# Performance work log

Hardware: AMD Instinct MI355X
Metric: run time of the kernel (lower is better)

## Reference

```python
import jax, jax.numpy as jnp
import numpy as np

N, F, P, E, HID = 50000, 4, 12, 1_600_000, 64  # nodes, input feats, periods (FH), edges, hidden


def setup_inputs() -> dict:
    key = jax.random.key(0)
    ks = jax.random.split(key, 16)

    def nrm(k, shp, scale=0.1):
        return jax.random.normal(k, shp, jnp.float32) * scale

    inp = {
        "x": jax.random.normal(ks[0], (N, F, P), jnp.float32),
        "edge_index": jax.random.randint(ks[1], (2, E), 0, N),
        "edge_weights": jax.random.uniform(ks[2], (E,), jnp.float32),
        "att": nrm(ks[3], (P,), 1.0),
    }
    i = 4
    for g in ("z", "r", "h"):  # TGCN gate params: GCNConv weight/bias + Linear(2*hid, hid)
        inp[f"Wg_{g}"] = nrm(ks[i], (F, HID))
        inp[f"bg_{g}"] = jnp.zeros((HID,), jnp.float32)
        inp[f"Wl_{g}"] = nrm(jax.random.fold_in(ks[i], 1), (2 * HID, HID))
        inp[f"bl_{g}"] = jnp.zeros((HID,), jnp.float32)
        i += 1
    for j in range(1, 5):
        inp[f"W{j}"] = nrm(ks[i], (HID, HID))
        inp[f"b{j}"] = jnp.zeros((HID,), jnp.float32)
        i += 1
    inp["Wo"] = nrm(ks[i], (HID, P * F))
    inp["bo"] = jnp.zeros((P * F,), jnp.float32)
    return inp


def _gcn_norm(edge_index, ew):
    # GCNConv default: add self loops (weight 1), symmetric D^-1/2 (A+I) D^-1/2 normalization
    src, dst = edge_index[0], edge_index[1]
    loop = jnp.arange(N)
    src_f = jnp.concatenate([src, loop])
    dst_f = jnp.concatenate([dst, loop])
    ew_f = jnp.concatenate([ew, jnp.ones((N,), ew.dtype)])
    deg = jax.ops.segment_sum(ew_f, dst_f, num_segments=N)
    dinv = jnp.where(deg > 0, jax.lax.rsqrt(deg), 0.0)
    norm = dinv[src_f] * ew_f * dinv[dst_f]
    return src_f, dst_f, norm


def _gcn(x, W, b, src, dst, norm):
    xw = x @ W                               # [N, HID] transform before propagate
    msg = xw[src] * norm[:, None]            # gather + scale, [E+N, HID]
    return jax.ops.segment_sum(msg, dst, num_segments=N) + b


def reference(x, edge_index, edge_weights, att,
              Wg_z, bg_z, Wl_z, bl_z,
              Wg_r, bg_r, Wl_r, bl_r,
              Wg_h, bg_h, Wl_h, bl_h,
              W1, b1, W2, b2, W3, b3, W4, b4, Wo, bo):
    src, dst, norm = _gcn_norm(edge_index, edge_weights)

    def tgcn_cell(xt):
        # A3TGCN passes H=None every period -> H starts at zeros each period
        Hz = jnp.zeros((xt.shape[0], HID), xt.dtype)
        z = jax.nn.sigmoid(jnp.concatenate([_gcn(xt, Wg_z, bg_z, src, dst, norm), Hz], -1) @ Wl_z + bl_z)
        r = jax.nn.sigmoid(jnp.concatenate([_gcn(xt, Wg_r, bg_r, src, dst, norm), Hz], -1) @ Wl_r + bl_r)
        htil = jnp.tanh(jnp.concatenate([_gcn(xt, Wg_h, bg_h, src, dst, norm), Hz * r], -1) @ Wl_h + bl_h)
        return z * Hz + (1.0 - z) * htil

    probs = jax.nn.softmax(att)
    h = jnp.zeros((N, HID), x.dtype)
    for p in range(P):  # small fixed period loop keeps peak memory at one period's messages
        h = h + probs[p] * tgcn_cell(x[:, :, p])

    h = jax.nn.relu(h)
    h = h @ W1 + b1
    h = h @ W2 + b2
    h = h @ W3 + b3
    h = h @ W4 + b4
    h = h @ Wo + bo                          # [N, FH*F]
    return h.reshape(-1, F, P)
```

## Files before the change

### kernel.cpp

```cpp
#include <hip/hip_runtime.h>
#include <hip/hip_fp16.h>

#define FP 48
#define HID 64
#define NP 12
#define PL 65
#define NBLK 256
#define CAPB 9216

__device__ __forceinline__ void mm_stage(const float* __restrict__ Alds,
                                         const float* __restrict__ Wg,
                                         float* __restrict__ Clds, int t)
{
    const int rg = (t >> 4) * 4, cg = (t & 15) * 4;
    float acc[4][4] = {};
    for (int k = 0; k < 64; ++k) {
        float a0 = Alds[(rg + 0) * PL + k];
        float a1 = Alds[(rg + 1) * PL + k];
        float a2 = Alds[(rg + 2) * PL + k];
        float a3 = Alds[(rg + 3) * PL + k];
        const float4 bv = *reinterpret_cast<const float4*>(Wg + k * 64 + cg);
        acc[0][0] += a0 * bv.x; acc[0][1] += a0 * bv.y; acc[0][2] += a0 * bv.z; acc[0][3] += a0 * bv.w;
        acc[1][0] += a1 * bv.x; acc[1][1] += a1 * bv.y; acc[1][2] += a1 * bv.z; acc[1][3] += a1 * bv.w;
        acc[2][0] += a2 * bv.x; acc[2][1] += a2 * bv.y; acc[2][2] += a2 * bv.z; acc[2][3] += a2 * bv.w;
        acc[3][0] += a3 * bv.x; acc[3][1] += a3 * bv.y; acc[3][2] += a3 * bv.z; acc[3][3] += a3 * bv.w;
    }
    for (int i = 0; i < 4; ++i)
        for (int j = 0; j < 4; ++j)
            Clds[(rg + i) * PL + cg + j] = acc[i][j];
}

__device__ __forceinline__ void bias_stage(const float* __restrict__ bin,
                                           const float* __restrict__ Wg,
                                           const float* __restrict__ badd,
                                           float* __restrict__ bout, int t)
{
    if (t < 64) {
        float s = badd[t];
        for (int k = 0; k < 64; ++k) s += bin[k] * Wg[k * 64 + t];
        bout[t] = s;
    }
}

__device__ void do_prep(
    const float* __restrict__ att,
    const float* __restrict__ Wg_z, const float* __restrict__ bg_z,
    const float* __restrict__ Wl_z, const float* __restrict__ bl_z,
    const float* __restrict__ Wg_h, const float* __restrict__ bg_h,
    const float* __restrict__ Wl_h, const float* __restrict__ bl_h,
    const float* __restrict__ W1, const float* __restrict__ b1,
    const float* __restrict__ W2, const float* __restrict__ b2,
    const float* __restrict__ W3, const float* __restrict__ b3,
    const float* __restrict__ W4, const float* __restrict__ b4,
    const float* __restrict__ Wo, const float* __restrict__ bo,
    float* __restrict__ probs, float* __restrict__ Mz, float* __restrict__ cz,
    float* __restrict__ Mh, float* __restrict__ ch,
    float* __restrict__ Wc, float* __restrict__ bc, int t)
{
    __shared__ float A[64 * PL];
    __shared__ float B[64 * PL];
    __shared__ float bias[64];
    __shared__ float bias2[64];

    if (t == 0) {
        float m = att[0];
        for (int p = 1; p < NP; ++p) m = fmaxf(m, att[p]);
        float e[NP]; float s = 0.f;
        for (int p = 0; p < NP; ++p) { e[p] = __expf(att[p] - m); s += e[p]; }
        float inv = 1.f / s;
        for (int p = 0; p < NP; ++p) probs[p] = e[p] * inv;
    }

    {
        int f = t >> 6, j = t & 63;
        float az = 0.f, ah = 0.f;
        for (int k = 0; k < HID; ++k) {
            az += Wg_z[f * HID + k] * Wl_z[k * HID + j];
            ah += Wg_h[f * HID + k] * Wl_h[k * HID + j];
        }
        Mz[t] = az; Mh[t] = ah;
    }
    if (t < HID) {
        float az = bl_z[t], ah = bl_h[t];
        for (int k = 0; k < HID; ++k) {
            az += bg_z[k] * Wl_z[k * HID + t];
            ah += bg_h[k] * Wl_h[k * HID + t];
        }
        cz[t] = az; ch[t] = ah;
    }

    for (int idx = t; idx < 4096; idx += 256) {
        int i = idx >> 6, j = idx & 63;
        A[i * PL + j] = W1[idx];
    }
    if (t < 64) bias[t] = b1[t];
    __syncthreads();

    mm_stage(A, W2, B, t);
    bias_stage(bias, W2, b2, bias2, t);
    __syncthreads();
    mm_stage(B, W3, A, t);
    bias_stage(bias2, W3, b3, bias, t);
    __syncthreads();
    mm_stage(A, W4, B, t);
    bias_stage(bias, W4, b4, bias2, t);
    __syncthreads();

    const int rg = (t >> 4) * 4, cg = (t & 15) * 4;
    if (cg < FP) {
        float acc[4][4] = {};
        for (int k = 0; k < 64; ++k) {
            float a0 = B[(rg + 0) * PL + k];
            float a1 = B[(rg + 1) * PL + k];
            float a2 = B[(rg + 2) * PL + k];
            float a3 = B[(rg + 3) * PL + k];
            const float4 bv = *reinterpret_cast<const float4*>(Wo + k * FP + cg);
            acc[0][0] += a0 * bv.x; acc[0][1] += a0 * bv.y; acc[0][2] += a0 * bv.z; acc[0][3] += a0 * bv.w;
            acc[1][0] += a1 * bv.x; acc[1][1] += a1 * bv.y; acc[1][2] += a1 * bv.z; acc[1][3] += a1 * bv.w;
            acc[2][0] += a2 * bv.x; acc[2][1] += a2 * bv.y; acc[2][2] += a2 * bv.z; acc[2][3] += a2 * bv.w;
            acc[3][0] += a3 * bv.x; acc[3][1] += a3 * bv.y; acc[3][2] += a3 * bv.z; acc[3][3] += a3 * bv.w;
        }
        for (int i = 0; i < 4; ++i)
            for (int j = 0; j < 4; ++j)
                Wc[(rg + i) * FP + cg + j] = acc[i][j];
    }
    if (t < FP) {
        float s = bo[t];
        for (int k = 0; k < 64; ++k) s += bias2[k] * Wo[k * FP + t];
        bc[t] = s;
    }
}

__global__ __launch_bounds__(256) void build_kernel(
    const int* __restrict__ src, const int* __restrict__ dst,
    const float* __restrict__ ew,
    unsigned* __restrict__ cursor, int2* __restrict__ binned,
    int E, int CE, int NBUK,
    const float* __restrict__ att,
    const float* __restrict__ Wg_z, const float* __restrict__ bg_z,
    const float* __restrict__ Wl_z, const float* __restrict__ bl_z,
    const float* __restrict__ Wg_h, const float* __restrict__ bg_h,
    const float* __restrict__ Wl_h, const float* __restrict__ bl_h,
    const float* __restrict__ W1, const float* __restrict__ b1,
    const float* __restrict__ W2, const float* __restrict__ b2,
    const float* __restrict__ W3, const float* __restrict__ b3,
    const float* __restrict__ W4, const float* __restrict__ b4,
    const float* __restrict__ Wo, const float* __restrict__ bo,
    float* __restrict__ probs, float* __restrict__ Mz, float* __restrict__ cz,
    float* __restrict__ Mh, float* __restrict__ ch,
    float* __restrict__ Wc, float* __restrict__ bc)
{
    const int t = threadIdx.x;
    if (blockIdx.x == NBLK) {
        do_prep(att, Wg_z, bg_z, Wl_z, bl_z, Wg_h, bg_h, Wl_h, bl_h,
                W1, b1, W2, b2, W3, b3, W4, b4, Wo, bo,
                probs, Mz, cz, Mh, ch, Wc, bc, t);
        return;
    }
    __shared__ int cnt[256];
    __shared__ int off[256];
    for (int i = t; i < NBUK; i += 256) cnt[i] = 0;
    __syncthreads();
    const int base = blockIdx.x * CE;
    const int endb = min(base + CE, E);
    for (int e = base + t; e < endb; e += 256)
        atomicAdd(&cnt[((unsigned)dst[e]) >> 8], 1);
    __syncthreads();
    for (int i = t; i < NBUK; i += 256)
        off[i] = (int)atomicAdd(&cursor[i], (unsigned)cnt[i]);
    __syncthreads();
    for (int e = base + t; e < endb; e += 256) {
        const int d = dst[e];
        const int b = ((unsigned)d) >> 8;
        const int r = atomicAdd(&off[b], 1);
        if (r < CAPB)
            binned[(size_t)b * CAPB + r] =
                make_int2(((d & 255) << 16) | src[e], __float_as_int(ew[e]));
    }
}

__global__ __launch_bounds__(256) void csr_convert_kernel(
    const int2* __restrict__ binned, const unsigned* __restrict__ cursor,
    unsigned* __restrict__ csr, int2* __restrict__ nodeinfo,
    const float* __restrict__ x,
    unsigned short* __restrict__ xs, int N, int NBUK)
{
    const int t = threadIdx.x;
    const int b = blockIdx.x;
    const int node0 = b << 8;
    const int nend = min(256, N - node0);
    const int ebeg = b * CAPB;
    const int ecnt = min((int)cursor[b], CAPB);
    const int eend = ebeg + ecnt;

    __shared__ int   cnt[256];
    __shared__ float fsum[256];
    __shared__ int   pfx[256];
    __shared__ float sdi[256];

    cnt[t] = 0; fsum[t] = 0.f;
    __syncthreads();

    for (int e = ebeg + t; e < eend; e += 256) {
        const int2 v = binned[e];
        const int dl = (v.x >> 16) & 255;
        atomicAdd(&cnt[dl], 1);
        atomicAdd(&fsum[dl], __int_as_float(v.y));
    }
    __syncthreads();

    const int myc = cnt[t];
    pfx[t] = myc;
    __syncthreads();
    for (int off = 1; off < 256; off <<= 1) {
        int tmp = (t >= off) ? pfx[t - off] : 0;
        __syncthreads();
        pfx[t] += tmp;
        __syncthreads();
    }
    const int excl = pfx[t] - myc;

    const float di = rsqrtf(1.f + fsum[t]);
    sdi[t] = di;
    if (t < nend)
        nodeinfo[node0 + t] = make_int2((myc << 22) | (ebeg + excl), __float_as_int(di));

    cnt[t] = ebeg + excl;
    __syncthreads();

    for (int e = ebeg + t; e < eend; e += 256) {
        const int2 v = binned[e];
        const int dl = (v.x >> 16) & 255;
        const int pos = atomicAdd(&cnt[dl], 1);
        const float w = __int_as_float(v.y);
        const unsigned hb = (unsigned)__half_as_ushort(__float2half_rn(w));
        csr[pos] = (unsigned)(v.x & 0xffff) | (hb << 16);
    }

    const int gtot = nend * 6;
    for (int g = t; g < gtot; g += 256) {
        const int nl = g / 6;
        const int q = g - nl * 6;
        const float dsc = sdi[nl];
        const float* xr = x + (size_t)(node0 + nl) * FP + q * 8;
        const float4 v0 = *reinterpret_cast<const float4*>(xr);
        const float4 v1 = *reinterpret_cast<const float4*>(xr + 4);
        unsigned p0 = (unsigned)__half_as_ushort(__float2half_rn(dsc * v0.x)) |
                      ((unsigned)__half_as_ushort(__float2half_rn(dsc * v0.y)) << 16);
        unsigned p1 = (unsigned)__half_as_ushort(__float2half_rn(dsc * v0.z)) |
                      ((unsigned)__half_as_ushort(__float2half_rn(dsc * v0.w)) << 16);
        unsigned p2 = (unsigned)__half_as_ushort(__float2half_rn(dsc * v1.x)) |
                      ((unsigned)__half_as_ushort(__float2half_rn(dsc * v1.y)) << 16);
        unsigned p3 = (unsigned)__half_as_ushort(__float2half_rn(dsc * v1.z)) |
                      ((unsigned)__half_as_ushort(__float2half_rn(dsc * v1.w)) << 16);
        *reinterpret_cast<int4*>(xs + (size_t)(node0 + nl) * FP + q * 8) =
            make_int4((int)p0, (int)p1, (int)p2, (int)p3);
    }
}

__global__ __launch_bounds__(256) void gather_node_kernel(
    const unsigned short* __restrict__ xs, const float* __restrict__ x,
    const int2* __restrict__ nodeinfo,
    const unsigned* __restrict__ csr,
    const float* __restrict__ probs,
    const float* __restrict__ Mz, const float* __restrict__ cz,
    const float* __restrict__ Mh, const float* __restrict__ ch,
    const float* __restrict__ Wc, const float* __restrict__ bc,
    float* __restrict__ out, int N)
{
    __shared__ __align__(16) float sWc[HID * FP];
    __shared__ __align__(16) float sprobs[16];
    __shared__ __align__(16) float yacc[4][384];
    __shared__ __align__(16) float yld[4][FP];
    __shared__ __align__(16) float hld[4][HID];
    for (int i = threadIdx.x; i < HID * FP; i += 256) sWc[i] = Wc[i];
    if (threadIdx.x < NP) sprobs[threadIdx.x] = probs[threadIdx.x];
    __syncthreads();

    const int lane = threadIdx.x & 63;
    const int wib  = threadIdx.x >> 6;
    const int n    = blockIdx.x * 4 + wib;
    if (n >= N) return;

    const int slot = lane >> 3;
    const int q    = lane & 7;
    const bool act = (q < 6);
    const int qc   = act ? q : 5;
    const char* xsb = (const char*)xs;

    const int2 ni = nodeinfo[n];
    const int beg = ni.x & 0x3FFFFF;
    const int end = beg + ((unsigned)ni.x >> 22);
    const float di = __int_as_float(ni.y);

    float a0 = 0.f, a1 = 0.f, a2 = 0.f, a3 = 0.f;
    float a4 = 0.f, a5 = 0.f, a6 = 0.f, a7 = 0.f;
    #pragma unroll 2
    for (int e = beg + slot; e < end; e += 8) {
        const unsigned ev = csr[e];
        const float w = __half2float(__ushort_as_half((unsigned short)(ev >> 16)));
        const unsigned soff = (ev & 0xffffu) * 96u;
        const int4 xv = *reinterpret_cast<const int4*>(xsb + soff + (qc << 4));
        const float2 f0 = __half22float2(*reinterpret_cast<const __half2*>(&xv.x));
        const float2 f1 = __half22float2(*reinterpret_cast<const __half2*>(&xv.y));
        const float2 f2 = __half22float2(*reinterpret_cast<const __half2*>(&xv.z));
        const float2 f3 = __half22float2(*reinterpret_cast<const __half2*>(&xv.w));
        a0 = fmaf(w, f0.x, a0); a1 = fmaf(w, f0.y, a1);
        a2 = fmaf(w, f1.x, a2); a3 = fmaf(w, f1.y, a3);
        a4 = fmaf(w, f2.x, a4); a5 = fmaf(w, f2.y, a5);
        a6 = fmaf(w, f3.x, a6); a7 = fmaf(w, f3.y, a7);
    }

    if (act) {
        float* dst0 = &yacc[wib][slot * 48 + q * 8];
        *reinterpret_cast<float4*>(dst0)     = make_float4(a0, a1, a2, a3);
        *reinterpret_cast<float4*>(dst0 + 4) = make_float4(a4, a5, a6, a7);
    }

    if (lane < FP) {
        const float* yf = yacc[wib];
        float s = 0.f;
        #pragma unroll
        for (int sl = 0; sl < 8; ++sl) s += yf[sl * 48 + lane];
        float xself = x[(size_t)n * FP + lane];
        float yv = di * s + di * di * xself;
        int f = lane / 12;
        int p = lane - f * 12;
        yld[wib][p * 4 + f] = yv;
    }

    const float mz0 = Mz[lane], mz1 = Mz[64 + lane], mz2 = Mz[128 + lane], mz3 = Mz[192 + lane];
    const float mh0 = Mh[lane], mh1 = Mh[64 + lane], mh2 = Mh[128 + lane], mh3 = Mh[192 + lane];
    const float czv = cz[lane], chv = ch[lane];
    const int   c   = (lane < FP) ? lane : 0;
    const float bcv = bc[c];

    const float* yw = yld[wib];
    float hacc = 0.f;
    #pragma unroll
    for (int p = 0; p < NP; ++p) {
        const float4 v = *reinterpret_cast<const float4*>(yw + p * 4);
        float az = czv + v.x * mz0 + v.y * mz1 + v.z * mz2 + v.w * mz3;
        float ah = chv + v.x * mh0 + v.y * mh1 + v.z * mh2 + v.w * mh3;
        float g  = __builtin_amdgcn_rcpf(1.f + __expf(az));
        float ahc = fminf(fmaxf(ah, -15.f), 15.f);
        float eh = __expf(2.f * ahc);
        float th = 1.f - 2.f * __builtin_amdgcn_rcpf(eh + 1.f);
        hacc += sprobs[p] * g * th;
    }
    hacc = fmaxf(hacc, 0.f);

    hld[wib][lane] = hacc;
    const float* hw = hld[wib];
    float o = bcv;
    #pragma unroll
    for (int i4 = 0; i4 < 16; ++i4) {
        const float4 h4 = *reinterpret_cast<const float4*>(hw + i4 * 4);
        o += h4.x * sWc[(i4 * 4 + 0) * FP + c];
        o += h4.y * sWc[(i4 * 4 + 1) * FP + c];
        o += h4.z * sWc[(i4 * 4 + 2) * FP + c];
        o += h4.w * sWc[(i4 * 4 + 3) * FP + c];
    }
    if (lane < FP) out[(size_t)n * FP + lane] = o;
}

extern "C" void kernel_launch(void* const* d_in, const int* in_sizes, int n_in,
                              void* d_out, int out_size, void* d_ws, size_t ws_size,
                              hipStream_t stream)
{
    const int N = in_sizes[0] / FP;
    const int E = in_sizes[1] / 2;
    const int NBUK = (N + 255) >> 8;
    const int CE = (E + NBLK - 1) / NBLK;

    const float* x    = (const float*)d_in[0];
    const int*   ei   = (const int*)d_in[1];
    const float* ew   = (const float*)d_in[2];
    const float* att  = (const float*)d_in[3];
    const float* Wg_z = (const float*)d_in[4];
    const float* bg_z = (const float*)d_in[5];
    const float* Wl_z = (const float*)d_in[6];
    const float* bl_z = (const float*)d_in[7];
    const float* Wg_h = (const float*)d_in[12];
    const float* bg_h = (const float*)d_in[13];
    const float* Wl_h = (const float*)d_in[14];
    const float* bl_h = (const float*)d_in[15];
    const float* W1 = (const float*)d_in[16]; const float* b1 = (const float*)d_in[17];
    const float* W2 = (const float*)d_in[18]; const float* b2 = (const float*)d_in[19];
    const float* W3 = (const float*)d_in[20]; const float* b3 = (const float*)d_in[21];
    const float* W4 = (const float*)d_in[22]; const float* b4 = (const float*)d_in[23];
    const float* Wo = (const float*)d_in[24]; const float* bo = (const float*)d_in[25];

    const int* srcp = ei;
    const int* dstp = ei + E;

    int2* binned       = (int2*)d_ws;
    unsigned* csr      = (unsigned*)(binned + (size_t)NBUK * CAPB);
    unsigned short* xs = (unsigned short*)(csr + (size_t)NBUK * CAPB);
    unsigned* cursor   = (unsigned*)(xs + (size_t)N * FP);
    int2* nodeinfo     = (int2*)(cursor + 256);
    float* probs       = (float*)(nodeinfo + N);
    float* Mz          = probs + 16;
    float* cz          = Mz + 256;
    float* Mh          = cz + 64;
    float* ch          = Mh + 256;
    float* Wc          = ch + 64;
    float* bc          = Wc + HID * FP;

    hipMemsetAsync(cursor, 0, (size_t)NBUK * sizeof(unsigned), stream);

    build_kernel<<<NBLK + 1, 256, 0, stream>>>(
        srcp, dstp, ew, cursor, binned, E, CE, NBUK,
        att, Wg_z, bg_z, Wl_z, bl_z, Wg_h, bg_h, Wl_h, bl_h,
        W1, b1, W2, b2, W3, b3, W4, b4, Wo, bo,
        probs, Mz, cz, Mh, ch, Wc, bc);

    csr_convert_kernel<<<NBUK, 256, 0, stream>>>(binned, cursor, csr, nodeinfo,
                                                 x, xs, N, NBUK);

    gather_node_kernel<<<(N + 3) / 4, 256, 0, stream>>>(xs, x, nodeinfo, csr,
                                                        probs, Mz, cz, Mh, ch, Wc, bc,
                                                        (float*)d_out, N);
}
```

Measured before the change: 252.2 us.

## Widen edge binning and CSR convert grids, use fma_mix in gather loop

The edge-binning kernel now runs over 1024 blocks instead of 256, and skips cursor atomics for empty buckets. The CSR-convert kernel runs 1024 threads per block, with the per-node scan limited to the first 256 threads. The gather loop replaces separate half-to-float conversions with inline v_fma_mix_f32 instructions that multiply packed fp16 features by the fp16 edge weight directly. These changes aim to raise parallelism in the preprocessing stages, since CSR convert has only about 196 blocks, and to cut ALU work per edge. In exchange there are more global cursor atomics and inline assembly that depends on the target ISA.

```diff
diff --git a/kernel.cpp b/kernel.cpp
--- a/kernel.cpp
+++ b/kernel.cpp
@@ -5,7 +5,7 @@
 #define HID 64
 #define NP 12
 #define PL 65
-#define NBLK 256
+#define NBB 1024
 #define CAPB 9216
 
 __device__ __forceinline__ void mm_stage(const float* __restrict__ Alds,
@@ -151,7 +151,7 @@
     float* __restrict__ Wc, float* __restrict__ bc)
 {
     const int t = threadIdx.x;
-    if (blockIdx.x == NBLK) {
+    if (blockIdx.x == NBB) {
         do_prep(att, Wg_z, bg_z, Wl_z, bl_z, Wg_h, bg_h, Wl_h, bl_h,
                 W1, b1, W2, b2, W3, b3, W4, b4, Wo, bo,
                 probs, Mz, cz, Mh, ch, Wc, bc, t);
@@ -159,15 +159,17 @@
     }
     __shared__ int cnt[256];
     __shared__ int off[256];
-    for (int i = t; i < NBUK; i += 256) cnt[i] = 0;
-    __syncthreads();
     const int base = blockIdx.x * CE;
     const int endb = min(base + CE, E);
+    cnt[t] = 0;
+    __syncthreads();
     for (int e = base + t; e < endb; e += 256)
         atomicAdd(&cnt[((unsigned)dst[e]) >> 8], 1);
     __syncthreads();
-    for (int i = t; i < NBUK; i += 256)
-        off[i] = (int)atomicAdd(&cursor[i], (unsigned)cnt[i]);
+    if (t < NBUK) {
+        const int c = cnt[t];
+        off[t] = c ? (int)atomicAdd(&cursor[t], (unsigned)c) : 0;
+    }
     __syncthreads();
     for (int e = base + t; e < endb; e += 256) {
         const int d = dst[e];
@@ -179,7 +181,7 @@
     }
 }
 
-__global__ __launch_bounds__(256) void csr_convert_kernel(
+__global__ __launch_bounds__(1024) void csr_convert_kernel(
     const int2* __restrict__ binned, const unsigned* __restrict__ cursor,
     unsigned* __restrict__ csr, int2* __restrict__ nodeinfo,
     const float* __restrict__ x,
@@ -198,10 +200,10 @@
     __shared__ int   pfx[256];
     __shared__ float sdi[256];
 
-    cnt[t] = 0; fsum[t] = 0.f;
-    __syncthreads();
-
-    for (int e = ebeg + t; e < eend; e += 256) {
+    if (t < 256) { cnt[t] = 0; fsum[t] = 0.f; }
+    __syncthreads();
+
+    for (int e = ebeg + t; e < eend; e += 1024) {
         const int2 v = binned[e];
         const int dl = (v.x >> 16) & 255;
         atomicAdd(&cnt[dl], 1);
@@ -209,26 +211,27 @@
     }
     __syncthreads();
 
-    const int myc = cnt[t];
-    pfx[t] = myc;
+    const int myc = (t < 256) ? cnt[t] : 0;
+    if (t < 256) pfx[t] = myc;
     __syncthreads();
     for (int off = 1; off < 256; off <<= 1) {
-        int tmp = (t >= off) ? pfx[t - off] : 0;
+        int tmp = (t >= off && t < 256) ? pfx[t - off] : 0;
         __syncthreads();
-        pfx[t] += tmp;
+        if (t < 256) pfx[t] += tmp;
         __syncthreads();
     }
-    const int excl = pfx[t] - myc;
-
-    const float di = rsqrtf(1.f + fsum[t]);
-    sdi[t] = di;
-    if (t < nend)
-        nodeinfo[node0 + t] = make_int2((myc << 22) | (ebeg + excl), __float_as_int(di));
-
-    cnt[t] = ebeg + excl;
-    __syncthreads();
-
-    for (int e = ebeg + t; e < eend; e += 256) {
+
+    if (t < 256) {
+        const int excl = pfx[t] - myc;
+        const float di = rsqrtf(1.f + fsum[t]);
+        sdi[t] = di;
+        if (t < nend)
+            nodeinfo[node0 + t] = make_int2((myc << 22) | (ebeg + excl), __float_as_int(di));
+        cnt[t] = ebeg + excl;
+    }
+    __syncthreads();
+
+    for (int e = ebeg + t; e < eend; e += 1024) {
         const int2 v = binned[e];
         const int dl = (v.x >> 16) & 255;
         const int pos = atomicAdd(&cnt[dl], 1);
@@ -238,7 +241,7 @@
     }
 
     const int gtot = nend * 6;
-    for (int g = t; g < gtot; g += 256) {
+    for (int g = t; g < gtot; g += 1024) {
         const int nl = g / 6;
         const int q = g - nl * 6;
         const float dsc = sdi[nl];
@@ -258,6 +261,13 @@
     }
 }
 
+#define FMAMIX_LO(acc, xpk, evw) \
+    asm("v_fma_mix_f32 %0, %1, %2, %0 op_sel:[0,1,0] op_sel_hi:[1,1,0]" \
+        : "+v"(acc) : "v"(xpk), "v"(evw))
+#define FMAMIX_HI(acc, xpk, evw) \
+    asm("v_fma_mix_f32 %0, %1, %2, %0 op_sel:[1,1,0] op_sel_hi:[1,1,0]" \
+        : "+v"(acc) : "v"(xpk), "v"(evw))
+
 __global__ __launch_bounds__(256) void gather_node_kernel(
     const unsigned short* __restrict__ xs, const float* __restrict__ x,
     const int2* __restrict__ nodeinfo,
@@ -290,7 +300,7 @@
 
     const int2 ni = nodeinfo[n];
     const int beg = ni.x & 0x3FFFFF;
-    const int end = beg + ((unsigned)ni.x >> 22);
+    const int end = beg + (int)((unsigned)ni.x >> 22);
     const float di = __int_as_float(ni.y);
 
     float a0 = 0.f, a1 = 0.f, a2 = 0.f, a3 = 0.f;
@@ -298,17 +308,12 @@
     #pragma unroll 2
     for (int e = beg + slot; e < end; e += 8) {
         const unsigned ev = csr[e];
-        const float w = __half2float(__ushort_as_half((unsigned short)(ev >> 16)));
         const unsigned soff = (ev & 0xffffu) * 96u;
         const int4 xv = *reinterpret_cast<const int4*>(xsb + soff + (qc << 4));
-        const float2 f0 = __half22float2(*reinterpret_cast<const __half2*>(&xv.x));
-        const float2 f1 = __half22float2(*reinterpret_cast<const __half2*>(&xv.y));
-        const float2 f2 = __half22float2(*reinterpret_cast<const __half2*>(&xv.z));
-        const float2 f3 = __half22float2(*reinterpret_cast<const __half2*>(&xv.w));
-        a0 = fmaf(w, f0.x, a0); a1 = fmaf(w, f0.y, a1);
-        a2 = fmaf(w, f1.x, a2); a3 = fmaf(w, f1.y, a3);
-        a4 = fmaf(w, f2.x, a4); a5 = fmaf(w, f2.y, a5);
-        a6 = fmaf(w, f3.x, a6); a7 = fmaf(w, f3.y, a7);
+        FMAMIX_LO(a0, xv.x, ev); FMAMIX_HI(a1, xv.x, ev);
+        FMAMIX_LO(a2, xv.y, ev); FMAMIX_HI(a3, xv.y, ev);
+        FMAMIX_LO(a4, xv.z, ev); FMAMIX_HI(a5, xv.z, ev);
+        FMAMIX_LO(a6, xv.w, ev); FMAMIX_HI(a7, xv.w, ev);
     }
 
     if (act) {
@@ -371,7 +376,7 @@
     const int N = in_sizes[0] / FP;
     const int E = in_sizes[1] / 2;
     const int NBUK = (N + 255) >> 8;
-    const int CE = (E + NBLK - 1) / NBLK;
+    const int CE = (E + NBB - 1) / NBB;
 
     const float* x    = (const float*)d_in[0];
     const int*   ei   = (const int*)d_in[1];
@@ -409,14 +414,14 @@
 
     hipMemsetAsync(cursor, 0, (size_t)NBUK * sizeof(unsigned), stream);
 
-    build_kernel<<<NBLK + 1, 256, 0, stream>>>(
+    build_kernel<<<NBB + 1, 256, 0, stream>>>(
         srcp, dstp, ew, cursor, binned, E, CE, NBUK,
         att, Wg_z, bg_z, Wl_z, bl_z, Wg_h, bg_h, Wl_h, bl_h,
         W1, b1, W2, b2, W3, b3, W4, b4, Wo, bo,
         probs, Mz, cz, Mh, ch, Wc, bc);
 
-    csr_convert_kernel<<<NBUK, 256, 0, stream>>>(binned, cursor, csr, nodeinfo,
-                                                 x, xs, N, NBUK);
+    csr_convert_kernel<<<NBUK, 1024, 0, stream>>>(binned, cursor, csr, nodeinfo,
+                                                  x, xs, N, NBUK);
 
     gather_node_kernel<<<(N + 3) / 4, 256, 0, stream>>>(xs, x, nodeinfo, csr,
                                                         probs, Mz, cz, Mh, ch, Wc, bc,
```

Result: slower. 273.8 us (+8.6%).
